# Performance work log

Hardware: AMD Instinct MI355X
Metric: run time of the kernel (lower is better)

Reference implementation:

```python
import jax, jax.numpy as jnp
import numpy as np

N, LMAX, E, H, P, F, HEADS, RD, R = 16384, 16, 128, 128, 128, 256, 8, 32, 64
DH = E // HEADS  # per-head dim


def _mlp2(x, W1, b1, W2, b2):
    # Linear -> ReLU -> Linear -> ReLU (matches nn.Sequential in lane/phase/fusion MLPs)
    return jax.nn.relu(jax.nn.relu(x @ W1 + b1) @ W2 + b2)


def setup_inputs() -> dict:
    key = jax.random.key(0)
    ks = iter(jax.random.split(key, 48))

    def nrm(shape, scale=0.05):
        return jax.random.normal(next(ks), shape, dtype=jnp.float32) * scale

    inp = {
        'queues': jax.random.uniform(next(ks), (N, LMAX), dtype=jnp.float32),
        'waits': jax.random.uniform(next(ks), (N, LMAX), dtype=jnp.float32),
        'phase_onehot': jax.random.uniform(next(ks), (N, 4), dtype=jnp.float32),
        'elapsed': jax.random.uniform(next(ks), (N,), dtype=jnp.float32),
        # ragged lane counts per TLS, clamped to >= 1 so every TLS has lanes
        'lane_counts': jnp.clip(jax.random.randint(next(ks), (N,), 0, 17), 1, LMAX).astype(jnp.int32),
        'region_ids': jax.random.randint(next(ks), (N,), 0, R).astype(jnp.int32),
        # lane_mlp: Linear(3,H), Linear(H,E)
        'W1': nrm((3, H)), 'b1': nrm((H,)),
        'W2': nrm((H, E)), 'b2': nrm((E,)),
        # MultiheadAttention in/out projections
        'Wq': nrm((E, E)), 'bq': nrm((E,)),
        'Wk': nrm((E, E)), 'bk': nrm((E,)),
        'Wv': nrm((E, E)), 'bv': nrm((E,)),
        'Wo': nrm((E, E)), 'bo': nrm((E,)),
        # phase_mlp: Linear(5,P), Linear(P,P)
        'Wp1': nrm((5, P)), 'bp1': nrm((P,)),
        'Wp2': nrm((P, P)), 'bp2': nrm((P,)),
        # region embedding table
        'region_table': nrm((R, RD), 1.0),
        # fusion_mlp: Linear(E+P+RD, F), Linear(F, F)
        'Wf1': nrm((E + P + RD, F)), 'bf1': nrm((F,)),
        'Wf2': nrm((F, F)), 'bf2': nrm((F,)),
        # heads
        'Wm': nrm((F, 1)), 'bm': nrm((1,)),
        'Wval': nrm((F, 1)), 'bval': nrm((1,)),
        'log_std': jnp.full((1,), float(np.log(0.3)), dtype=jnp.float32),
    }
    return inp


def reference(queues, waits, phase_onehot, elapsed, lane_counts, region_ids,
              W1, b1, W2, b2, Wq, bq, Wk, bk, Wv, bv, Wo, bo,
              Wp1, bp1, Wp2, bp2, region_table, Wf1, bf1, Wf2, bf2,
              Wm, bm, Wval, bval, log_std):
    # lane features [N, L, 3] = (queue, wait, elapsed)
    lane_feats = jnp.stack(
        [queues, waits, jnp.broadcast_to(elapsed[:, None], queues.shape)], axis=-1)
    lane_emb = _mlp2(lane_feats, W1, b1, W2, b2)  # [N, L, E]

    # batched multi-head self-attention over lanes, key-masked for ragged L
    q = (lane_emb @ Wq + bq).reshape(N, LMAX, HEADS, DH)
    k = (lane_emb @ Wk + bk).reshape(N, LMAX, HEADS, DH)
    v = (lane_emb @ Wv + bv).reshape(N, LMAX, HEADS, DH)
    scores = jnp.einsum('nqhd,nkhd->nhqk', q, k) / jnp.sqrt(jnp.float32(DH))
    lane_mask = jnp.arange(LMAX)[None, :] < lane_counts[:, None]  # [N, L]
    scores = jnp.where(lane_mask[:, None, None, :], scores, jnp.float32(-1e9))
    attn = jax.nn.softmax(scores, axis=-1)
    ctx = jnp.einsum('nhqk,nkhd->nqhd', attn, v).reshape(N, LMAX, E)
    attn_out = ctx @ Wo + bo  # [N, L, E]

    # mean over the true L lanes per TLS (matches attn_out.mean(dim=1) on exact L)
    denom = lane_counts.astype(jnp.float32)[:, None]
    lane_context = jnp.sum(attn_out * lane_mask[:, :, None], axis=1) / denom  # [N, E]

    phase_feat = jnp.concatenate([phase_onehot, elapsed[:, None]], axis=-1)  # [N, 5]
    phase_emb = _mlp2(phase_feat, Wp1, bp1, Wp2, bp2)  # [N, P]

    region_emb = region_table[region_ids]  # [N, RD]

    fused = jnp.concatenate([lane_context, phase_emb, region_emb], axis=-1)
    h = _mlp2(fused, Wf1, bf1, Wf2, bf2)  # [N, F]

    means = (h @ Wm + bm)[:, 0]    # [N]
    values = (h @ Wval + bval)[:, 0]  # [N]
    log_std_b = jnp.broadcast_to(log_std, means.shape)  # [N]
    return means, log_std_b, values
```

## Files before the change

### kernel.cpp

```cpp
#include <hip/hip_runtime.h>
#include <hip/hip_bf16.h>
#include <stdint.h>

#define NTLS 16384

typedef float f32x4 __attribute__((ext_vector_type(4)));
typedef short bf16x8 __attribute__((ext_vector_type(8)));
typedef short bf16x4 __attribute__((ext_vector_type(4)));

__device__ __forceinline__ unsigned pk2(float a, float b){
    unsigned r;
    asm("v_cvt_pk_bf16_f32 %0, %1, %2" : "=v"(r) : "v"(a), "v"(b));
    return r;
}
__device__ __forceinline__ short f2bf(float x){
    return (short)(pk2(x, 0.f) & 0xffff);
}
__device__ __forceinline__ unsigned lds_lo(const void* p){
    return (unsigned)(size_t)p;
}
__device__ __forceinline__ bf16x4 ds_tr(unsigned addr){
    bf16x4 d;
    asm volatile("ds_read_b64_tr_b16 %0, %1" : "=v"(d) : "v"(addr) : "memory");
    return d;
}
__device__ __forceinline__ void lgkm0(){
    asm volatile("s_waitcnt lgkmcnt(0)" ::: "memory");
    __builtin_amdgcn_sched_barrier(0);
}
__device__ __forceinline__ void gload4_wait(const short* base,
        bf16x8& d0, bf16x8& d1, bf16x8& d2, bf16x8& d3){
    asm volatile(
        "global_load_dwordx4 %0, %4, off\n\t"
        "global_load_dwordx4 %1, %4, off offset:1024\n\t"
        "global_load_dwordx4 %2, %4, off offset:2048\n\t"
        "global_load_dwordx4 %3, %4, off offset:3072\n\t"
        "s_waitcnt vmcnt(0)"
        : "=&v"(d0), "=&v"(d1), "=&v"(d2), "=&v"(d3)
        : "v"(base)
        : "memory");
}
__device__ __forceinline__ bf16x8 cat44(bf16x4 lo, bf16x4 hi){
    bf16x8 r;
    r[0]=lo[0]; r[1]=lo[1]; r[2]=lo[2]; r[3]=lo[3];
    r[4]=hi[0]; r[5]=hi[1]; r[6]=hi[2]; r[7]=hi[3];
    return r;
}
__device__ __forceinline__ bf16x8 cat40(bf16x4 lo){
    bf16x8 r;
    r[0]=lo[0]; r[1]=lo[1]; r[2]=lo[2]; r[3]=lo[3];
    r[4]=0; r[5]=0; r[6]=0; r[7]=0;
    return r;
}
#define MFMA16(a,b,c) __builtin_amdgcn_mfma_f32_16x16x32_bf16((a),(b),(c),0,0,0)

__global__ __launch_bounds__(256) void prepack(
    const float* __restrict__ W2, const float* __restrict__ Wq,
    const float* __restrict__ Wk, const float* __restrict__ Wv,
    const float* __restrict__ Wo, const float* __restrict__ Wp2,
    const float* __restrict__ Wf1, const float* __restrict__ Wf2,
    short* __restrict__ out)
{
    int gid = blockIdx.x * 256 + threadIdx.x;
    const float* src; short* dst; int K, Nn; int id = gid;
    if (id < 12288){
        int wsel = id >> 11; id &= 2047;
        const float* tab[6] = {W2, Wq, Wk, Wv, Wo, Wp2};
        src = tab[wsel]; dst = out + wsel * 16384; K = 128; Nn = 128;
    } else if (id < 21504){
        id -= 12288; src = Wf1; dst = out + 98304; K = 288; Nn = 256;
    } else {
        id -= 21504; src = Wf2; dst = out + 172032; K = 256; Nn = 256;
    }
    int lane = id & 63, f = id >> 6;
    int KT = K >> 5;
    int nt = f / KT, kt = f - nt * KT;
    int n  = nt * 16 + (lane & 15);
    int kb = kt * 32 + 4 * (lane >> 4);
    unsigned w0 = pk2(src[(kb+0)*Nn+n],  src[(kb+1)*Nn+n]);
    unsigned w1 = pk2(src[(kb+2)*Nn+n],  src[(kb+3)*Nn+n]);
    unsigned w2 = pk2(src[(kb+16)*Nn+n], src[(kb+17)*Nn+n]);
    unsigned w3 = pk2(src[(kb+18)*Nn+n], src[(kb+19)*Nn+n]);
    *(uint4*)&dst[(f*64+lane)*8] = make_uint4(w0,w1,w2,w3);
}

__global__ __launch_bounds__(512, 4) void k1_lane(
    const float* __restrict__ queues, const float* __restrict__ waits,
    const float* __restrict__ elapsed, const int* __restrict__ lane_counts,
    const float* __restrict__ W1, const float* __restrict__ b1,
    const float* __restrict__ b2,
    const float* __restrict__ bq, const float* __restrict__ bk_, const float* __restrict__ bv_,
    const short* __restrict__ wpk,
    short* __restrict__ meanb)
{
    const int tid  = threadIdx.x;
    const int w    = tid >> 6, lane = tid & 63;
    const int nl   = lane & 15, kb = lane >> 4;
    const int base = blockIdx.x << 3;

    __shared__ __align__(512) short s_h1[8*2048];
    __shared__ __align__(512) short s_emb[8*2048];

    const unsigned trofs = (unsigned)(kb*128 + nl*8);
    const short* Wpk2 = wpk;
    const short* WpkQ = wpk + 16384;
    const short* WpkK = wpk + 32768;
    const short* WpkV = wpk + 49152;

    {
        const int n = base + w;
        const float ev = elapsed[n];
        float qv = queues[n*16 + nl];
        float wv = waits [n*16 + nl];
        float qm[4], wmv[4];
        #pragma unroll
        for (int r = 0; r < 4; ++r){
            qm[r]  = __shfl(qv, 4*kb + r, 16);
            wmv[r] = __shfl(wv, 4*kb + r, 16);
        }
        #pragma unroll
        for (int i = 0; i < 8; ++i){
            int c = nl + 16*i;
            float w0 = W1[c], w1 = W1[128+c], w2 = W1[256+c], bb = b1[c];
            float v0 = fmaxf(fmaf(qm[0], w0, fmaf(wmv[0], w1, fmaf(ev, w2, bb))), 0.f);
            float v1 = fmaxf(fmaf(qm[1], w0, fmaf(wmv[1], w1, fmaf(ev, w2, bb))), 0.f);
            float v2 = fmaxf(fmaf(qm[2], w0, fmaf(wmv[2], w1, fmaf(ev, w2, bb))), 0.f);
            float v3 = fmaxf(fmaf(qm[3], w0, fmaf(wmv[3], w1, fmaf(ev, w2, bb))), 0.f);
            *(uint2*)&s_h1[w*2048 + c*16 + 4*kb] = make_uint2(pk2(v0,v1), pk2(v2,v3));
        }
    }
    __syncthreads();

    {
        bf16x8 B2[4];
        gload4_wait(Wpk2 + ((w*4)*64 + lane)*8, B2[0], B2[1], B2[2], B2[3]);
        const int c0 = 16*w + nl;
        const float bb0 = b2[c0];
        for (int t = 0; t < 8; ++t){
            unsigned ab = lds_lo(s_h1) + t*4096 + trofs;
            bf16x4 tr[8];
            #pragma unroll
            for (int kt = 0; kt < 4; ++kt){
                tr[2*kt]   = ds_tr(ab + kt*1024);
                tr[2*kt+1] = ds_tr(ab + kt*1024 + 512);
            }
            lgkm0();
            f32x4 a0 = {0.f,0.f,0.f,0.f};
            #pragma unroll
            for (int kt = 0; kt < 4; ++kt)
                a0 = MFMA16(cat44(tr[2*kt], tr[2*kt+1]), B2[kt], a0);
            *(uint2*)&s_emb[t*2048 + c0*16 + 4*kb] =
                make_uint2(pk2(fmaxf(a0[0]+bb0,0.f), fmaxf(a0[1]+bb0,0.f)),
                           pk2(fmaxf(a0[2]+bb0,0.f), fmaxf(a0[3]+bb0,0.f)));
        }
    }
    __syncthreads();

    {
        bf16x8 BQ[4], BK[4], BV[4];
        gload4_wait(WpkQ + ((w*4)*64 + lane)*8, BQ[0], BQ[1], BQ[2], BQ[3]);
        gload4_wait(WpkK + ((w*4)*64 + lane)*8, BK[0], BK[1], BK[2], BK[3]);
        gload4_wait(WpkV + ((w*4)*64 + lane)*8, BV[0], BV[1], BV[2], BV[3]);
        const int c0 = 16*w + nl;
        const float xq = bq[c0], xk = bk_[c0], xv = bv_[c0];
        short* wbuf = s_h1 + w*2048;
        const f32x4 zero = {0.f,0.f,0.f,0.f};

        for (int t = 0; t < 8; ++t){
            const int n = base + t;
            const int L = lane_counts[n];
            const float invL = 1.f / (float)L;

            unsigned ab = lds_lo(s_emb) + t*4096 + trofs;
            bf16x4 tr[8];
            #pragma unroll
            for (int kt = 0; kt < 4; ++kt){
                tr[2*kt]   = ds_tr(ab + kt*1024);
                tr[2*kt+1] = ds_tr(ab + kt*1024 + 512);
            }
            lgkm0();
            f32x4 q0=zero, k0=zero, v0=zero;
            #pragma unroll
            for (int kt = 0; kt < 4; ++kt){
                bf16x8 A = cat44(tr[2*kt], tr[2*kt+1]);
                q0 = MFMA16(A, BQ[kt], q0);
                k0 = MFMA16(A, BK[kt], k0);
                v0 = MFMA16(A, BV[kt], v0);
            }
            short* buf = wbuf + (t&1)*1024;
            *(uint2*)&buf[nl*16 + 4*kb] =
                make_uint2(pk2(q0[0]+xq, q0[1]+xq), pk2(q0[2]+xq, q0[3]+xq));
            *(uint2*)&buf[256 + nl*16 + 4*kb] =
                make_uint2(pk2(k0[0]+xk, k0[1]+xk), pk2(k0[2]+xk, k0[3]+xk));
            *(uint2*)&buf[512 + nl*16 + 4*kb] =
                make_uint2(pk2(v0[0]+xv, v0[1]+xv), pk2(v0[2]+xv, v0[3]+xv));
            lgkm0();

            const unsigned ba = lds_lo(buf);
            bf16x4 qf = ds_tr(ba + trofs);
            bf16x4 kf = ds_tr(ba + 512 + trofs);
            bf16x4 vf = *(const bf16x4*)&buf[512 + nl*16 + 4*kb];
            lgkm0();

            f32x4 st = MFMA16(cat40(kf), cat40(qf), zero);
            float pr[4], ps = 0.f;
            #pragma unroll
            for (int r = 0; r < 4; ++r){
                pr[r] = (4*kb+r < L) ? __expf(st[r]*0.25f) : 0.f;
                ps += pr[r];
            }
            ps += __shfl_xor(ps, 16);
            ps += __shfl_xor(ps, 32);
            float inv = 1.f/ps;
            union { bf16x8 v; unsigned u[4]; } P;
            P.u[0] = pk2(pr[0]*inv, pr[1]*inv);
            P.u[1] = pk2(pr[2]*inv, pr[3]*inv);
            P.u[2] = 0; P.u[3] = 0;
            f32x4 ctx = MFMA16(P.v, cat40(vf), zero);
            float pm = 0.f;
            #pragma unroll
            for (int r = 0; r < 4; ++r) if (4*kb+r < L) pm += ctx[r];
            pm += __shfl_xor(pm, 16);
            pm += __shfl_xor(pm, 32);
            if (kb == 0)
                meanb[((n>>4)<<11) + c0*16 + (n&15)] = f2bf(pm * invL);
        }
    }
}

__global__ __launch_bounds__(256, 2) void k2_tail(
    const float* __restrict__ phase_onehot, const float* __restrict__ elapsed,
    const int* __restrict__ region_ids, const float* __restrict__ region_table,
    const float* __restrict__ Wp1, const float* __restrict__ bp1, const float* __restrict__ bp2,
    const float* __restrict__ bo,
    const float* __restrict__ bf1, const float* __restrict__ bf2_,
    const float* __restrict__ Wm, const float* __restrict__ bm,
    const float* __restrict__ Wval, const float* __restrict__ bval,
    const float* __restrict__ log_std,
    const short* __restrict__ wpk, const short* __restrict__ meanb,
    float* __restrict__ out)
{
    const int tid  = threadIdx.x;
    const int w    = tid >> 6, lane = tid & 63;
    const int nl   = lane & 15, kb = lane >> 4;
    const int base = blockIdx.x << 5;

    __shared__ __align__(512) short s_mean[2*2048];
    __shared__ __align__(512) short s_ph1[2*2048];
    __shared__ __align__(512) short s_fused[2*4608];
    __shared__ __align__(512) short s_hf[2*4096];
    __shared__ float s_part[4][2][16][2];

    const unsigned trofs = (unsigned)(kb*128 + nl*8);
    const bf16x8* WpkO  = (const bf16x8*)(wpk + 65536);
    const bf16x8* WpkP2 = (const bf16x8*)(wpk + 81920);
    const bf16x8* WpkF1 = (const bf16x8*)(wpk + 98304);
    const bf16x8* WpkF2 = (const bf16x8*)(wpk + 172032);

    {
        const uint4* src = (const uint4*)(meanb + base*128);
        uint4* dst = (uint4*)s_mean;
        dst[tid]       = src[tid];
        dst[256 + tid] = src[256 + tid];
    }
    {
        const int r = tid >> 3, cb = tid & 7, n = base + r;
        const float p0 = phase_onehot[n*4+0], p1 = phase_onehot[n*4+1];
        const float p2 = phase_onehot[n*4+2], p3 = phase_onehot[n*4+3];
        const float ev = elapsed[n];
        #pragma unroll
        for (int jc = 0; jc < 16; ++jc){
            int c = cb*16 + jc;
            float a = fmaf(p0, Wp1[c], fmaf(p1, Wp1[128+c], fmaf(p2, Wp1[256+c],
                      fmaf(p3, Wp1[384+c], fmaf(ev, Wp1[512+c], bp1[c])))));
            s_ph1[(r>>4)*2048 + c*16 + (r&15)] = f2bf(fmaxf(a, 0.f));
        }
        const int rid = region_ids[n];
        #pragma unroll
        for (int jc = 0; jc < 4; ++jc){
            int c = (tid&7)*4 + jc;
            s_fused[(r>>4)*4608 + (256+c)*16 + (r&15)] = f2bf(region_table[rid*32 + c]);
        }
    }
    __syncthreads();

    {
        bf16x8 BO[8], BP[8];
        #pragma unroll
        for (int nt2 = 0; nt2 < 2; ++nt2)
            #pragma unroll
            for (int kt = 0; kt < 4; ++kt){
                int fi = ((2*w+nt2)*4+kt)*64 + lane;
                BO[nt2*4+kt] = WpkO[fi];
                BP[nt2*4+kt] = WpkP2[fi];
            }
        const int c0 = 32*w + nl, c1 = c0 + 16;
        const float o0b = bo[c0], o1b = bo[c1];
        const float p0b = bp2[c0], p1b = bp2[c1];
        #pragma unroll
        for (int mt = 0; mt < 2; ++mt){
            unsigned am = lds_lo(s_mean) + mt*4096 + trofs;
            unsigned ap = lds_lo(s_ph1)  + mt*4096 + trofs;
            bf16x4 t[16];
            #pragma unroll
            for (int kt = 0; kt < 4; ++kt){
                t[2*kt]     = ds_tr(am + kt*1024);
                t[2*kt+1]   = ds_tr(am + kt*1024 + 512);
                t[8+2*kt]   = ds_tr(ap + kt*1024);
                t[9+2*kt]   = ds_tr(ap + kt*1024 + 512);
            }
            lgkm0();
            f32x4 o0={0.f,0.f,0.f,0.f}, o1=o0, p0=o0, p1=o0;
            #pragma unroll
            for (int kt = 0; kt < 4; ++kt){
                bf16x8 Am = cat44(t[2*kt],   t[2*kt+1]);
                bf16x8 Ap = cat44(t[8+2*kt], t[9+2*kt]);
                o0 = MFMA16(Am, BO[kt],   o0);
                o1 = MFMA16(Am, BO[4+kt], o1);
                p0 = MFMA16(Ap, BP[kt],   p0);
                p1 = MFMA16(Ap, BP[4+kt], p1);
            }
            short* fb = s_fused + mt*4608;
            *(uint2*)&fb[c0*16 + 4*kb] =
                make_uint2(pk2(o0[0]+o0b, o0[1]+o0b), pk2(o0[2]+o0b, o0[3]+o0b));
            *(uint2*)&fb[c1*16 + 4*kb] =
                make_uint2(pk2(o1[0]+o1b, o1[1]+o1b), pk2(o1[2]+o1b, o1[3]+o1b));
            *(uint2*)&fb[(128+c0)*16 + 4*kb] =
                make_uint2(pk2(fmaxf(p0[0]+p0b,0.f), fmaxf(p0[1]+p0b,0.f)),
                           pk2(fmaxf(p0[2]+p0b,0.f), fmaxf(p0[3]+p0b,0.f)));
            *(uint2*)&fb[(128+c1)*16 + 4*kb] =
                make_uint2(pk2(fmaxf(p1[0]+p1b,0.f), fmaxf(p1[1]+p1b,0.f)),
                           pk2(fmaxf(p1[2]+p1b,0.f), fmaxf(p1[3]+p1b,0.f)));
        }
    }
    __syncthreads();

    {
        bf16x8 A[2][9];
        #pragma unroll
        for (int mt = 0; mt < 2; ++mt){
            unsigned ab = lds_lo(s_fused) + mt*9216 + trofs;
            bf16x4 t[18];
            #pragma unroll
            for (int kt = 0; kt < 9; ++kt){
                t[2*kt]   = ds_tr(ab + kt*1024);
                t[2*kt+1] = ds_tr(ab + kt*1024 + 512);
            }
            lgkm0();
            #pragma unroll
            for (int kt = 0; kt < 9; ++kt) A[mt][kt] = cat44(t[2*kt], t[2*kt+1]);
        }
        #pragma unroll
        for (int nt2 = 0; nt2 < 4; ++nt2){
            const int nt = 4*w + nt2;
            bf16x8 Bf[9];
            #pragma unroll
            for (int kt = 0; kt < 9; ++kt) Bf[kt] = WpkF1[(nt*9+kt)*64 + lane];
            f32x4 a0 = {0.f,0.f,0.f,0.f}, a1 = a0;
            #pragma unroll
            for (int kt = 0; kt < 9; ++kt){
                a0 = MFMA16(A[0][kt], Bf[kt], a0);
                a1 = MFMA16(A[1][kt], Bf[kt], a1);
            }
            const int c = nt*16 + nl;
            const float bb = bf1[c];
            *(uint2*)&s_hf[c*16 + 4*kb] =
                make_uint2(pk2(fmaxf(a0[0]+bb,0.f), fmaxf(a0[1]+bb,0.f)),
                           pk2(fmaxf(a0[2]+bb,0.f), fmaxf(a0[3]+bb,0.f)));
            *(uint2*)&s_hf[4096 + c*16 + 4*kb] =
                make_uint2(pk2(fmaxf(a1[0]+bb,0.f), fmaxf(a1[1]+bb,0.f)),
                           pk2(fmaxf(a1[2]+bb,0.f), fmaxf(a1[3]+bb,0.f)));
        }
    }
    __syncthreads();

    {
        bf16x8 A[2][8];
        #pragma unroll
        for (int mt = 0; mt < 2; ++mt){
            unsigned ab = lds_lo(s_hf) + mt*8192 + trofs;
            bf16x4 t[16];
            #pragma unroll
            for (int kt = 0; kt < 8; ++kt){
                t[2*kt]   = ds_tr(ab + kt*1024);
                t[2*kt+1] = ds_tr(ab + kt*1024 + 512);
            }
            lgkm0();
            #pragma unroll
            for (int kt = 0; kt < 8; ++kt) A[mt][kt] = cat44(t[2*kt], t[2*kt+1]);
        }
        float sm0[4] = {0,0,0,0}, sv0[4] = {0,0,0,0};
        float sm1[4] = {0,0,0,0}, sv1[4] = {0,0,0,0};
        #pragma unroll
        for (int nt2 = 0; nt2 < 4; ++nt2){
            const int nt = 4*w + nt2;
            bf16x8 Bf[8];
            #pragma unroll
            for (int kt = 0; kt < 8; ++kt) Bf[kt] = WpkF2[(nt*8+kt)*64 + lane];
            f32x4 a0 = {0.f,0.f,0.f,0.f}, a1 = a0;
            #pragma unroll
            for (int kt = 0; kt < 8; ++kt){
                a0 = MFMA16(A[0][kt], Bf[kt], a0);
                a1 = MFMA16(A[1][kt], Bf[kt], a1);
            }
            const int c = nt*16 + nl;
            const float bb = bf2_[c], wm = Wm[c], wv = Wval[c];
            #pragma unroll
            for (int r = 0; r < 4; ++r){
                float h0 = fmaxf(a0[r]+bb, 0.f);
                float h1 = fmaxf(a1[r]+bb, 0.f);
                sm0[r] = fmaf(h0, wm, sm0[r]);  sv0[r] = fmaf(h0, wv, sv0[r]);
                sm1[r] = fmaf(h1, wm, sm1[r]);  sv1[r] = fmaf(h1, wv, sv1[r]);
            }
        }
        #pragma unroll
        for (int off = 1; off < 16; off <<= 1){
            #pragma unroll
            for (int r = 0; r < 4; ++r){
                sm0[r] += __shfl_xor(sm0[r], off);  sv0[r] += __shfl_xor(sv0[r], off);
                sm1[r] += __shfl_xor(sm1[r], off);  sv1[r] += __shfl_xor(sv1[r], off);
            }
        }
        if (nl == 0){
            #pragma unroll
            for (int r = 0; r < 4; ++r){
                s_part[w][0][4*kb+r][0] = sm0[r];  s_part[w][0][4*kb+r][1] = sv0[r];
                s_part[w][1][4*kb+r][0] = sm1[r];  s_part[w][1][4*kb+r][1] = sv1[r];
            }
        }
    }
    __syncthreads();

    if (tid < 32){
        const int r = tid, n = base + r;
        float sm = bm[0], sv = bval[0];
        #pragma unroll
        for (int ww = 0; ww < 4; ++ww){
            sm += s_part[ww][r>>4][r&15][0];
            sv += s_part[ww][r>>4][r&15][1];
        }
        out[n]          = sm;
        out[NTLS + n]   = log_std[0];
        out[2*NTLS + n] = sv;
    }
}

extern "C" void kernel_launch(void* const* d_in, const int* in_sizes, int n_in,
                              void* d_out, int out_size, void* d_ws, size_t ws_size,
                              hipStream_t stream) {
    const float* queues       = (const float*)d_in[0];
    const float* waits        = (const float*)d_in[1];
    const float* phase_onehot = (const float*)d_in[2];
    const float* elapsed      = (const float*)d_in[3];
    const int*   lane_counts  = (const int*)d_in[4];
    const int*   region_ids   = (const int*)d_in[5];
    const float* W1  = (const float*)d_in[6];
    const float* b1  = (const float*)d_in[7];
    const float* W2  = (const float*)d_in[8];
    const float* b2  = (const float*)d_in[9];
    const float* Wq  = (const float*)d_in[10];
    const float* bq  = (const float*)d_in[11];
    const float* Wk  = (const float*)d_in[12];
    const float* bk  = (const float*)d_in[13];
    const float* Wv  = (const float*)d_in[14];
    const float* bv  = (const float*)d_in[15];
    const float* Wo  = (const float*)d_in[16];
    const float* bo  = (const float*)d_in[17];
    const float* Wp1 = (const float*)d_in[18];
    const float* bp1 = (const float*)d_in[19];
    const float* Wp2 = (const float*)d_in[20];
    const float* bp2 = (const float*)d_in[21];
    const float* region_table = (const float*)d_in[22];
    const float* Wf1 = (const float*)d_in[23];
    const float* bf1 = (const float*)d_in[24];
    const float* Wf2 = (const float*)d_in[25];
    const float* bf2 = (const float*)d_in[26];
    const float* Wm  = (const float*)d_in[27];
    const float* bm  = (const float*)d_in[28];
    const float* Wval = (const float*)d_in[29];
    const float* bval = (const float*)d_in[30];
    const float* log_std = (const float*)d_in[31];
    float* out = (float*)d_out;

    short* wpk   = (short*)d_ws;
    short* meanb = (short*)((char*)d_ws + 524288);

    prepack<<<116, 256, 0, stream>>>(W2, Wq, Wk, Wv, Wo, Wp2, Wf1, Wf2, wpk);
    k1_lane<<<2048, 512, 0, stream>>>(
        queues, waits, elapsed, lane_counts,
        W1, b1, b2, bq, bk, bv, wpk, meanb);
    k2_tail<<<512, 256, 0, stream>>>(
        phase_onehot, elapsed, region_ids, region_table,
        Wp1, bp1, bp2, bo, bf1, bf2, Wm, bm, Wval, bval, log_std,
        wpk, meanb, out);
}
```

Measured before the change: 190.0 us.

## Process TLS pairs in k1 attention loop and widen k2_tail to 512 threads

In k1_lane, the W2 and QKV/attention loops now handle two TLS items per iteration. This interleaves independent MFMA chains and LDS transposed reads so latency can be hidden within a wave. k2_tail is relaunched with 512 threads (8 waves): the Wo and Wp2 projections are split between wave groups, and the fusion MLP output tiles are spread over twice as many waves. The cost is higher register pressure in k1 and more per-block reduction slots in k2.

```diff
diff --git a/kernel.cpp b/kernel.cpp
--- a/kernel.cpp
+++ b/kernel.cpp
@@ -136,22 +136,32 @@
         gload4_wait(Wpk2 + ((w*4)*64 + lane)*8, B2[0], B2[1], B2[2], B2[3]);
         const int c0 = 16*w + nl;
         const float bb0 = b2[c0];
-        for (int t = 0; t < 8; ++t){
-            unsigned ab = lds_lo(s_h1) + t*4096 + trofs;
-            bf16x4 tr[8];
-            #pragma unroll
-            for (int kt = 0; kt < 4; ++kt){
-                tr[2*kt]   = ds_tr(ab + kt*1024);
-                tr[2*kt+1] = ds_tr(ab + kt*1024 + 512);
-            }
-            lgkm0();
-            f32x4 a0 = {0.f,0.f,0.f,0.f};
-            #pragma unroll
-            for (int kt = 0; kt < 4; ++kt)
-                a0 = MFMA16(cat44(tr[2*kt], tr[2*kt+1]), B2[kt], a0);
-            *(uint2*)&s_emb[t*2048 + c0*16 + 4*kb] =
-                make_uint2(pk2(fmaxf(a0[0]+bb0,0.f), fmaxf(a0[1]+bb0,0.f)),
-                           pk2(fmaxf(a0[2]+bb0,0.f), fmaxf(a0[3]+bb0,0.f)));
+        for (int tp = 0; tp < 4; ++tp){
+            unsigned abA = lds_lo(s_h1) + (2*tp)*4096 + trofs;
+            bf16x4 trA[8], trB[8];
+            #pragma unroll
+            for (int kt = 0; kt < 4; ++kt){
+                trA[2*kt]   = ds_tr(abA + kt*1024);
+                trA[2*kt+1] = ds_tr(abA + kt*1024 + 512);
+            }
+            #pragma unroll
+            for (int kt = 0; kt < 4; ++kt){
+                trB[2*kt]   = ds_tr(abA + 4096 + kt*1024);
+                trB[2*kt+1] = ds_tr(abA + 4096 + kt*1024 + 512);
+            }
+            lgkm0();
+            f32x4 aA = {0.f,0.f,0.f,0.f}, aB = {0.f,0.f,0.f,0.f};
+            #pragma unroll
+            for (int kt = 0; kt < 4; ++kt){
+                aA = MFMA16(cat44(trA[2*kt], trA[2*kt+1]), B2[kt], aA);
+                aB = MFMA16(cat44(trB[2*kt], trB[2*kt+1]), B2[kt], aB);
+            }
+            *(uint2*)&s_emb[(2*tp)*2048 + c0*16 + 4*kb] =
+                make_uint2(pk2(fmaxf(aA[0]+bb0,0.f), fmaxf(aA[1]+bb0,0.f)),
+                           pk2(fmaxf(aA[2]+bb0,0.f), fmaxf(aA[3]+bb0,0.f)));
+            *(uint2*)&s_emb[(2*tp+1)*2048 + c0*16 + 4*kb] =
+                make_uint2(pk2(fmaxf(aB[0]+bb0,0.f), fmaxf(aB[1]+bb0,0.f)),
+                           pk2(fmaxf(aB[2]+bb0,0.f), fmaxf(aB[3]+bb0,0.f)));
         }
     }
     __syncthreads();
@@ -164,71 +174,97 @@
         const int c0 = 16*w + nl;
         const float xq = bq[c0], xk = bk_[c0], xv = bv_[c0];
         short* wbuf = s_h1 + w*2048;
+        short* bufA = wbuf;
+        short* bufB = wbuf + 1024;
         const f32x4 zero = {0.f,0.f,0.f,0.f};
 
-        for (int t = 0; t < 8; ++t){
-            const int n = base + t;
-            const int L = lane_counts[n];
-            const float invL = 1.f / (float)L;
-
-            unsigned ab = lds_lo(s_emb) + t*4096 + trofs;
-            bf16x4 tr[8];
-            #pragma unroll
-            for (int kt = 0; kt < 4; ++kt){
-                tr[2*kt]   = ds_tr(ab + kt*1024);
-                tr[2*kt+1] = ds_tr(ab + kt*1024 + 512);
-            }
-            lgkm0();
-            f32x4 q0=zero, k0=zero, v0=zero;
-            #pragma unroll
-            for (int kt = 0; kt < 4; ++kt){
-                bf16x8 A = cat44(tr[2*kt], tr[2*kt+1]);
-                q0 = MFMA16(A, BQ[kt], q0);
-                k0 = MFMA16(A, BK[kt], k0);
-                v0 = MFMA16(A, BV[kt], v0);
-            }
-            short* buf = wbuf + (t&1)*1024;
-            *(uint2*)&buf[nl*16 + 4*kb] =
-                make_uint2(pk2(q0[0]+xq, q0[1]+xq), pk2(q0[2]+xq, q0[3]+xq));
-            *(uint2*)&buf[256 + nl*16 + 4*kb] =
-                make_uint2(pk2(k0[0]+xk, k0[1]+xk), pk2(k0[2]+xk, k0[3]+xk));
-            *(uint2*)&buf[512 + nl*16 + 4*kb] =
-                make_uint2(pk2(v0[0]+xv, v0[1]+xv), pk2(v0[2]+xv, v0[3]+xv));
-            lgkm0();
-
-            const unsigned ba = lds_lo(buf);
-            bf16x4 qf = ds_tr(ba + trofs);
-            bf16x4 kf = ds_tr(ba + 512 + trofs);
-            bf16x4 vf = *(const bf16x4*)&buf[512 + nl*16 + 4*kb];
-            lgkm0();
-
-            f32x4 st = MFMA16(cat40(kf), cat40(qf), zero);
-            float pr[4], ps = 0.f;
+        for (int tp = 0; tp < 4; ++tp){
+            const int nA = base + 2*tp, nB = nA + 1;
+            const int LA = lane_counts[nA], LB = lane_counts[nB];
+
+            unsigned abA = lds_lo(s_emb) + (2*tp)*4096 + trofs;
+            bf16x4 trA[8], trB[8];
+            #pragma unroll
+            for (int kt = 0; kt < 4; ++kt){
+                trA[2*kt]   = ds_tr(abA + kt*1024);
+                trA[2*kt+1] = ds_tr(abA + kt*1024 + 512);
+            }
+            #pragma unroll
+            for (int kt = 0; kt < 4; ++kt){
+                trB[2*kt]   = ds_tr(abA + 4096 + kt*1024);
+                trB[2*kt+1] = ds_tr(abA + 4096 + kt*1024 + 512);
+            }
+            lgkm0();
+            f32x4 qA=zero, kA2=zero, vA=zero, qB=zero, kB2=zero, vB=zero;
+            #pragma unroll
+            for (int kt = 0; kt < 4; ++kt){
+                bf16x8 EA = cat44(trA[2*kt], trA[2*kt+1]);
+                bf16x8 EB = cat44(trB[2*kt], trB[2*kt+1]);
+                qA  = MFMA16(EA, BQ[kt], qA);   qB  = MFMA16(EB, BQ[kt], qB);
+                kA2 = MFMA16(EA, BK[kt], kA2);  kB2 = MFMA16(EB, BK[kt], kB2);
+                vA  = MFMA16(EA, BV[kt], vA);   vB  = MFMA16(EB, BV[kt], vB);
+            }
+            *(uint2*)&bufA[nl*16 + 4*kb] =
+                make_uint2(pk2(qA[0]+xq, qA[1]+xq), pk2(qA[2]+xq, qA[3]+xq));
+            *(uint2*)&bufA[256 + nl*16 + 4*kb] =
+                make_uint2(pk2(kA2[0]+xk, kA2[1]+xk), pk2(kA2[2]+xk, kA2[3]+xk));
+            *(uint2*)&bufA[512 + nl*16 + 4*kb] =
+                make_uint2(pk2(vA[0]+xv, vA[1]+xv), pk2(vA[2]+xv, vA[3]+xv));
+            *(uint2*)&bufB[nl*16 + 4*kb] =
+                make_uint2(pk2(qB[0]+xq, qB[1]+xq), pk2(qB[2]+xq, qB[3]+xq));
+            *(uint2*)&bufB[256 + nl*16 + 4*kb] =
+                make_uint2(pk2(kB2[0]+xk, kB2[1]+xk), pk2(kB2[2]+xk, kB2[3]+xk));
+            *(uint2*)&bufB[512 + nl*16 + 4*kb] =
+                make_uint2(pk2(vB[0]+xv, vB[1]+xv), pk2(vB[2]+xv, vB[3]+xv));
+            lgkm0();
+
+            const unsigned baA = lds_lo(bufA), baB = lds_lo(bufB);
+            bf16x4 qfA = ds_tr(baA + trofs);
+            bf16x4 kfA = ds_tr(baA + 512 + trofs);
+            bf16x4 qfB = ds_tr(baB + trofs);
+            bf16x4 kfB = ds_tr(baB + 512 + trofs);
+            bf16x4 vfA = *(const bf16x4*)&bufA[512 + nl*16 + 4*kb];
+            bf16x4 vfB = *(const bf16x4*)&bufB[512 + nl*16 + 4*kb];
+            lgkm0();
+
+            f32x4 stA = MFMA16(cat40(kfA), cat40(qfA), zero);
+            f32x4 stB = MFMA16(cat40(kfB), cat40(qfB), zero);
+            float prA[4], psA = 0.f, prB[4], psB = 0.f;
             #pragma unroll
             for (int r = 0; r < 4; ++r){
-                pr[r] = (4*kb+r < L) ? __expf(st[r]*0.25f) : 0.f;
-                ps += pr[r];
-            }
-            ps += __shfl_xor(ps, 16);
-            ps += __shfl_xor(ps, 32);
-            float inv = 1.f/ps;
-            union { bf16x8 v; unsigned u[4]; } P;
-            P.u[0] = pk2(pr[0]*inv, pr[1]*inv);
-            P.u[1] = pk2(pr[2]*inv, pr[3]*inv);
-            P.u[2] = 0; P.u[3] = 0;
-            f32x4 ctx = MFMA16(P.v, cat40(vf), zero);
-            float pm = 0.f;
-            #pragma unroll
-            for (int r = 0; r < 4; ++r) if (4*kb+r < L) pm += ctx[r];
-            pm += __shfl_xor(pm, 16);
-            pm += __shfl_xor(pm, 32);
-            if (kb == 0)
-                meanb[((n>>4)<<11) + c0*16 + (n&15)] = f2bf(pm * invL);
-        }
-    }
-}
-
-__global__ __launch_bounds__(256, 2) void k2_tail(
+                prA[r] = (4*kb+r < LA) ? __expf(stA[r]*0.25f) : 0.f;
+                prB[r] = (4*kb+r < LB) ? __expf(stB[r]*0.25f) : 0.f;
+                psA += prA[r];  psB += prB[r];
+            }
+            psA += __shfl_xor(psA, 16);  psB += __shfl_xor(psB, 16);
+            psA += __shfl_xor(psA, 32);  psB += __shfl_xor(psB, 32);
+            const float invA = 1.f/psA, invB = 1.f/psB;
+            union { bf16x8 v; unsigned u[4]; } PA, PB;
+            PA.u[0] = pk2(prA[0]*invA, prA[1]*invA);
+            PA.u[1] = pk2(prA[2]*invA, prA[3]*invA);
+            PA.u[2] = 0; PA.u[3] = 0;
+            PB.u[0] = pk2(prB[0]*invB, prB[1]*invB);
+            PB.u[1] = pk2(prB[2]*invB, prB[3]*invB);
+            PB.u[2] = 0; PB.u[3] = 0;
+            f32x4 ctxA = MFMA16(PA.v, cat40(vfA), zero);
+            f32x4 ctxB = MFMA16(PB.v, cat40(vfB), zero);
+            float pmA = 0.f, pmB = 0.f;
+            #pragma unroll
+            for (int r = 0; r < 4; ++r){
+                if (4*kb+r < LA) pmA += ctxA[r];
+                if (4*kb+r < LB) pmB += ctxB[r];
+            }
+            pmA += __shfl_xor(pmA, 16);  pmB += __shfl_xor(pmB, 16);
+            pmA += __shfl_xor(pmA, 32);  pmB += __shfl_xor(pmB, 32);
+            if (kb == 0){
+                meanb[((nA>>4)<<11) + c0*16 + (nA&15)] = f2bf(pmA / (float)LA);
+                meanb[((nB>>4)<<11) + c0*16 + (nB&15)] = f2bf(pmB / (float)LB);
+            }
+        }
+    }
+}
+
+__global__ __launch_bounds__(512, 2) void k2_tail(
     const float* __restrict__ phase_onehot, const float* __restrict__ elapsed,
     const int* __restrict__ region_ids, const float* __restrict__ region_table,
     const float* __restrict__ Wp1, const float* __restrict__ bp1, const float* __restrict__ bp2,
@@ -249,7 +285,7 @@
     __shared__ __align__(512) short s_ph1[2*2048];
     __shared__ __align__(512) short s_fused[2*4608];
     __shared__ __align__(512) short s_hf[2*4096];
-    __shared__ float s_part[4][2][16][2];
+    __shared__ float s_part[8][2][16][2];
 
     const unsigned trofs = (unsigned)(kb*128 + nl*8);
     const bf16x8* WpkO  = (const bf16x8*)(wpk + 65536);
@@ -257,80 +293,67 @@
     const bf16x8* WpkF1 = (const bf16x8*)(wpk + 98304);
     const bf16x8* WpkF2 = (const bf16x8*)(wpk + 172032);
 
-    {
-        const uint4* src = (const uint4*)(meanb + base*128);
-        uint4* dst = (uint4*)s_mean;
-        dst[tid]       = src[tid];
-        dst[256 + tid] = src[256 + tid];
-    }
-    {
-        const int r = tid >> 3, cb = tid & 7, n = base + r;
+    ((uint4*)s_mean)[tid] = ((const uint4*)(meanb + base*128))[tid];
+    {
+        const int r = tid >> 4, cb = tid & 15, n = base + r;
         const float p0 = phase_onehot[n*4+0], p1 = phase_onehot[n*4+1];
         const float p2 = phase_onehot[n*4+2], p3 = phase_onehot[n*4+3];
         const float ev = elapsed[n];
         #pragma unroll
-        for (int jc = 0; jc < 16; ++jc){
-            int c = cb*16 + jc;
+        for (int jc = 0; jc < 8; ++jc){
+            int c = cb*8 + jc;
             float a = fmaf(p0, Wp1[c], fmaf(p1, Wp1[128+c], fmaf(p2, Wp1[256+c],
                       fmaf(p3, Wp1[384+c], fmaf(ev, Wp1[512+c], bp1[c])))));
             s_ph1[(r>>4)*2048 + c*16 + (r&15)] = f2bf(fmaxf(a, 0.f));
         }
         const int rid = region_ids[n];
-        #pragma unroll
-        for (int jc = 0; jc < 4; ++jc){
-            int c = (tid&7)*4 + jc;
-            s_fused[(r>>4)*4608 + (256+c)*16 + (r&15)] = f2bf(region_table[rid*32 + c]);
-        }
+        const int cc = cb*2;
+        s_fused[(r>>4)*4608 + (256+cc)*16 + (r&15)]   = f2bf(region_table[rid*32 + cc]);
+        s_fused[(r>>4)*4608 + (256+cc+1)*16 + (r&15)] = f2bf(region_table[rid*32 + cc + 1]);
     }
     __syncthreads();
 
     {
-        bf16x8 BO[8], BP[8];
-        #pragma unroll
-        for (int nt2 = 0; nt2 < 2; ++nt2)
-            #pragma unroll
-            for (int kt = 0; kt < 4; ++kt){
-                int fi = ((2*w+nt2)*4+kt)*64 + lane;
-                BO[nt2*4+kt] = WpkO[fi];
-                BP[nt2*4+kt] = WpkP2[fi];
-            }
-        const int c0 = 32*w + nl, c1 = c0 + 16;
-        const float o0b = bo[c0], o1b = bo[c1];
-        const float p0b = bp2[c0], p1b = bp2[c1];
+        const int g  = w >> 2;
+        const int q2 = w & 3;
+        const bf16x8* WB  = g ? WpkP2 : WpkO;
+        const short* Asrc = g ? s_ph1 : s_mean;
+        bf16x8 B[8];
+        #pragma unroll
+        for (int j = 0; j < 2; ++j)
+            #pragma unroll
+            for (int kt = 0; kt < 4; ++kt)
+                B[j*4+kt] = WB[((2*q2+j)*4+kt)*64 + lane];
         #pragma unroll
         for (int mt = 0; mt < 2; ++mt){
-            unsigned am = lds_lo(s_mean) + mt*4096 + trofs;
-            unsigned ap = lds_lo(s_ph1)  + mt*4096 + trofs;
-            bf16x4 t[16];
-            #pragma unroll
-            for (int kt = 0; kt < 4; ++kt){
-                t[2*kt]     = ds_tr(am + kt*1024);
-                t[2*kt+1]   = ds_tr(am + kt*1024 + 512);
-                t[8+2*kt]   = ds_tr(ap + kt*1024);
-                t[9+2*kt]   = ds_tr(ap + kt*1024 + 512);
-            }
-            lgkm0();
-            f32x4 o0={0.f,0.f,0.f,0.f}, o1=o0, p0=o0, p1=o0;
-            #pragma unroll
-            for (int kt = 0; kt < 4; ++kt){
-                bf16x8 Am = cat44(t[2*kt],   t[2*kt+1]);
-                bf16x8 Ap = cat44(t[8+2*kt], t[9+2*kt]);
-                o0 = MFMA16(Am, BO[kt],   o0);
-                o1 = MFMA16(Am, BO[4+kt], o1);
-                p0 = MFMA16(Ap, BP[kt],   p0);
-                p1 = MFMA16(Ap, BP[4+kt], p1);
-            }
-            short* fb = s_fused + mt*4608;
-            *(uint2*)&fb[c0*16 + 4*kb] =
-                make_uint2(pk2(o0[0]+o0b, o0[1]+o0b), pk2(o0[2]+o0b, o0[3]+o0b));
-            *(uint2*)&fb[c1*16 + 4*kb] =
-                make_uint2(pk2(o1[0]+o1b, o1[1]+o1b), pk2(o1[2]+o1b, o1[3]+o1b));
-            *(uint2*)&fb[(128+c0)*16 + 4*kb] =
-                make_uint2(pk2(fmaxf(p0[0]+p0b,0.f), fmaxf(p0[1]+p0b,0.f)),
-                           pk2(fmaxf(p0[2]+p0b,0.f), fmaxf(p0[3]+p0b,0.f)));
-            *(uint2*)&fb[(128+c1)*16 + 4*kb] =
-                make_uint2(pk2(fmaxf(p1[0]+p1b,0.f), fmaxf(p1[1]+p1b,0.f)),
-                           pk2(fmaxf(p1[2]+p1b,0.f), fmaxf(p1[3]+p1b,0.f)));
+            unsigned ab = lds_lo(Asrc) + mt*4096 + trofs;
+            bf16x4 t[8];
+            #pragma unroll
+            for (int kt = 0; kt < 4; ++kt){
+                t[2*kt]   = ds_tr(ab + kt*1024);
+                t[2*kt+1] = ds_tr(ab + kt*1024 + 512);
+            }
+            lgkm0();
+            bf16x8 A[4];
+            #pragma unroll
+            for (int kt = 0; kt < 4; ++kt) A[kt] = cat44(t[2*kt], t[2*kt+1]);
+            #pragma unroll
+            for (int j = 0; j < 2; ++j){
+                const int c = (2*q2+j)*16 + nl;
+                const float bb = g ? bp2[c] : bo[c];
+                f32x4 acc = {0.f,0.f,0.f,0.f};
+                #pragma unroll
+                for (int kt = 0; kt < 4; ++kt) acc = MFMA16(A[kt], B[j*4+kt], acc);
+                short* fb = s_fused + mt*4608 + (g ? (128+c)*16 : c*16);
+                if (g){
+                    *(uint2*)&fb[4*kb] =
+                        make_uint2(pk2(fmaxf(acc[0]+bb,0.f), fmaxf(acc[1]+bb,0.f)),
+                                   pk2(fmaxf(acc[2]+bb,0.f), fmaxf(acc[3]+bb,0.f)));
+                } else {
+                    *(uint2*)&fb[4*kb] =
+                        make_uint2(pk2(acc[0]+bb, acc[1]+bb), pk2(acc[2]+bb, acc[3]+bb));
+                }
+            }
         }
     }
     __syncthreads();
@@ -351,8 +374,8 @@
             for (int kt = 0; kt < 9; ++kt) A[mt][kt] = cat44(t[2*kt], t[2*kt+1]);
         }
         #pragma unroll
-        for (int nt2 = 0; nt2 < 4; ++nt2){
-            const int nt = 4*w + nt2;
+        for (int j = 0; j < 2; ++j){
+            const int nt = 2*w + j;
             bf16x8 Bf[9];
             #pragma unroll
             for (int kt = 0; kt < 9; ++kt) Bf[kt] = WpkF1[(nt*9+kt)*64 + lane];
@@ -392,8 +415,8 @@
         float sm0[4] = {0,0,0,0}, sv0[4] = {0,0,0,0};
         float sm1[4] = {0,0,0,0}, sv1[4] = {0,0,0,0};
         #pragma unroll
-        for (int nt2 = 0; nt2 < 4; ++nt2){
-            const int nt = 4*w + nt2;
+        for (int j = 0; j < 2; ++j){
+            const int nt = 2*w + j;
             bf16x8 Bf[8];
             #pragma unroll
             for (int kt = 0; kt < 8; ++kt) Bf[kt] = WpkF2[(nt*8+kt)*64 + lane];
@@ -435,7 +458,7 @@
         const int r = tid, n = base + r;
         float sm = bm[0], sv = bval[0];
         #pragma unroll
-        for (int ww = 0; ww < 4; ++ww){
+        for (int ww = 0; ww < 8; ++ww){
             sm += s_part[ww][r>>4][r&15][0];
             sv += s_part[ww][r>>4][r&15][1];
         }
@@ -489,7 +512,7 @@
     k1_lane<<<2048, 512, 0, stream>>>(
         queues, waits, elapsed, lane_counts,
         W1, b1, b2, bq, bk, bv, wpk, meanb);
-    k2_tail<<<512, 256, 0, stream>>>(
+    k2_tail<<<512, 512, 0, stream>>>(
         phase_onehot, elapsed, region_ids, region_table,
         Wp1, bp1, bp2, bo, bf1, bf2, Wm, bm, Wval, bval, log_std,
         wpk, meanb, out);
```

Result: no change. 188.4 us (-0.9%).
